# Kernel optimization log

Measured on AMD Instinct MI355X. Metric: run time of the kernel, lower is better.

Reference implementation:

```python
import jax, jax.numpy as jnp
import numpy as np

NUM_HEADS = 16


def setup_inputs() -> dict:
    key = jax.random.key(0)
    ks = jax.random.split(key, 7)
    B, S, H = 4, 2048, 1024
    scale = 1.0 / np.sqrt(H)
    return {
        "hidden_states": jax.random.normal(ks[0], (B, S, H), dtype=jnp.float32),
        "attention_mask": jnp.ones((B, S), dtype=jnp.int32),
        "Wq": jax.random.normal(ks[1], (H, H), dtype=jnp.float32) * scale,
        "bq": jnp.zeros((H,), dtype=jnp.float32),
        "Wk": jax.random.normal(ks[2], (H, H), dtype=jnp.float32) * scale,
        "bk": jnp.zeros((H,), dtype=jnp.float32),
        "Wv": jax.random.normal(ks[3], (H, H), dtype=jnp.float32) * scale,
        "bv": jnp.zeros((H,), dtype=jnp.float32),
    }


def _split_heads(x, n_heads):
    B, S, H = x.shape
    return x.reshape(B, S, n_heads, H // n_heads).transpose(0, 2, 1, 3)  # [B,h,S,d]


def reference(hidden_states, attention_mask, Wq, bq, Wk, bk, Wv, bv):
    B, S, H = hidden_states.shape
    dh = H // NUM_HEADS
    # nn.Linear applies x @ W.T + b
    q = _split_heads(hidden_states @ Wq.T + bq, NUM_HEADS)
    k = _split_heads(hidden_states @ Wk.T + bk, NUM_HEADS)
    v = _split_heads(hidden_states @ Wv.T + bv, NUM_HEADS)
    scores = jnp.einsum("bhqd,bhkd->bhqk", q, k)  # [B,h,S,S]
    # masked_fill with -inf before scaling == masking after scaling
    mask = attention_mask[:, None, None, :] == 0
    scores = jnp.where(mask, -jnp.inf, scores)
    probs = jax.nn.softmax(scores / jnp.sqrt(jnp.float32(dh)), axis=-1)
    out = jnp.einsum("bhqk,bhkd->bhqd", probs, v)  # [B,h,S,d]
    return out.transpose(0, 2, 1, 3).reshape(B, S, H)
```

## Files before the change

### kernel.cpp

```cpp
#include <hip/hip_runtime.h>
#include <hip/hip_bf16.h>
#include <stdint.h>

constexpr int CB  = 4;
constexpr int CS  = 2048;
constexpr int CH  = 1024;
constexpr int CNH = 16;
constexpr int CDH = 64;
constexpr int CM  = CB * CS;

typedef __bf16 bf16x8 __attribute__((ext_vector_type(8)));
typedef float  f32x4  __attribute__((ext_vector_type(4)));

__device__ __forceinline__ unsigned short f2bf(float f) {
    union { float f; unsigned u; } c; c.f = f;
    unsigned u = c.u;
    unsigned r = (u + 0x7fffu + ((u >> 16) & 1u)) >> 16;
    return (unsigned short)r;
}

__device__ __forceinline__ void gl_lds16(const void* g, void* l) {
    __builtin_amdgcn_global_load_lds((const __attribute__((address_space(1))) uint32_t*)g,
                                     (__attribute__((address_space(3))) uint32_t*)l,
                                     16, 0, 0);
}

__device__ __forceinline__ float fexp2(float x) {
#if __has_builtin(__builtin_amdgcn_exp2f)
    return __builtin_amdgcn_exp2f(x);
#else
    return exp2f(x);
#endif
}

__device__ __forceinline__ unsigned cvtpk_bf16(float lo, float hi) {
    unsigned r;
    asm("v_cvt_pk_bf16_f32 %0, %1, %2" : "=v"(r) : "v"(lo), "v"(hi));
    return r;
}

__device__ __forceinline__ void pl32swap(unsigned &a, unsigned &b) {
#if __has_builtin(__builtin_amdgcn_permlane32_swap)
    auto r = __builtin_amdgcn_permlane32_swap(a, b, false, false);
    a = r[0]; b = r[1];
#else
    int lane = threadIdx.x & 63;
    unsigned as = (unsigned)__shfl((int)a, lane ^ 32);
    unsigned bs = (unsigned)__shfl((int)b, lane ^ 32);
    unsigned na = (lane < 32) ? a : bs;
    unsigned nb = (lane < 32) ? as : b;
    a = na; b = nb;
#endif
}

__device__ __forceinline__ void pl16swap(unsigned &a, unsigned &b) {
#if __has_builtin(__builtin_amdgcn_permlane16_swap)
    auto r = __builtin_amdgcn_permlane16_swap(a, b, false, false);
    a = r[0]; b = r[1];
#else
    unsigned as = __builtin_amdgcn_ds_swizzle(a, 0x401F);
    unsigned bs = __builtin_amdgcn_ds_swizzle(b, 0x401F);
    int odd = (threadIdx.x >> 4) & 1;
    unsigned na = odd ? bs : a;
    unsigned nb = odd ? b : as;
    a = na; b = nb;
#endif
}

constexpr float C_SC = 0.125f * 1.44269504f;

__global__ __launch_bounds__(256) void cvt_all(const float* __restrict__ hs,
                                               const float* __restrict__ w0,
                                               const float* __restrict__ w1,
                                               const float* __restrict__ w2,
                                               unsigned short* __restrict__ Xb,
                                               unsigned short* __restrict__ Wb) {
    int z = blockIdx.y;
    const float* src; unsigned short* dst; int n4;
    if (z == 0)      { src = hs; dst = Xb;              n4 = CM * CH / 4; }
    else if (z == 1) { src = w0; dst = Wb;              n4 = CH * CH / 4; }
    else if (z == 2) { src = w1; dst = Wb + CH * CH;    n4 = CH * CH / 4; }
    else             { src = w2; dst = Wb + 2 * CH * CH; n4 = CH * CH / 4; }
    int i = blockIdx.x * blockDim.x + threadIdx.x;
    if (i < n4) {
        float4 v = ((const float4*)src)[i];
        ushort4 o;
        o.x = f2bf(v.x); o.y = f2bf(v.y); o.z = f2bf(v.z); o.w = f2bf(v.w);
        ((ushort4*)dst)[i] = o;
    }
}

__global__ __launch_bounds__(256) void qkv_gemm(
    const unsigned short* __restrict__ Xb,
    const unsigned short* __restrict__ Wb,
    const float* __restrict__ bq, const float* __restrict__ bk, const float* __restrict__ bv,
    unsigned short* __restrict__ Qo,
    unsigned short* __restrict__ Ko,
    unsigned short* __restrict__ Vt)
{
    __shared__ alignas(16) unsigned char smem[34816];
    typedef unsigned short (*tile_t)[128][32];
    tile_t As = (tile_t)smem;
    tile_t Bs = (tile_t)(smem + 16384);
    typedef unsigned short (*ep_t)[136];
    ep_t Ep = (ep_t)smem;

    const int tid  = threadIdx.x;
    const int wave = tid >> 6, lane = tid & 63;
    const int wm = wave >> 1, wn = wave & 1;
    const int col = lane & 15, quad = lane >> 4;
    const int gm = blockIdx.x * 128, gn = blockIdx.y * 128;
    const int z  = blockIdx.z;
    const unsigned short* W = Wb + (size_t)z * CH * CH;

    f32x4 zero = {0.f, 0.f, 0.f, 0.f};
    f32x4 acc[4][4];
    for (int i = 0; i < 4; i++) for (int j = 0; j < 4; j++) acc[i][j] = zero;

    const int arow = lane >> 2;
    const int acol = (lane & 3) * 8;

    auto stage = [&](int buf, int k0) {
        for (int c = 0; c < 2; ++c) {
            int r0 = wave * 32 + c * 16;
            gl_lds16(Xb + (size_t)(gm + r0 + arow) * CH + k0 + acol, &As[buf][r0][0]);
            gl_lds16(W  + (size_t)(gn + r0 + arow) * CH + k0 + acol, &Bs[buf][r0][0]);
        }
    };

    stage(0, 0);
    for (int kk = 0; kk < 32; ++kk) {
        int cur = kk & 1;
        __syncthreads();
        if (kk < 31) stage(cur ^ 1, (kk + 1) * 32);
        bf16x8 af[4], bfm[4];
        for (int i = 0; i < 4; i++)
            af[i] = *(const bf16x8*)&As[cur][wm * 64 + i * 16 + col][quad * 8];
        for (int j = 0; j < 4; j++)
            bfm[j] = *(const bf16x8*)&Bs[cur][wn * 64 + j * 16 + col][quad * 8];
        for (int i = 0; i < 4; i++)
            for (int j = 0; j < 4; j++)
                acc[i][j] = __builtin_amdgcn_mfma_f32_16x16x32_bf16(af[i], bfm[j], acc[i][j], 0, 0, 0);
    }

    __syncthreads();

    const float* bias = (z == 0) ? bq : (z == 1) ? bk : bv;
    const int bb = gm >> 11, ss0 = gm & 2047;
    const int h0 = gn >> 6;

    if (z == 2) {
        for (int j = 0; j < 4; j++) {
            int nl = wn * 64 + j * 16 + col;
            float bias_v = bias[gn + nl];
            for (int i = 0; i < 4; i++) {
                int ml = wm * 64 + i * 16 + quad * 4;
                unsigned d0 = (unsigned)f2bf(acc[i][j][0] + bias_v) |
                              ((unsigned)f2bf(acc[i][j][1] + bias_v) << 16);
                unsigned d1 = (unsigned)f2bf(acc[i][j][2] + bias_v) |
                              ((unsigned)f2bf(acc[i][j][3] + bias_v) << 16);
                *(unsigned*)&Ep[nl][ml]     = d0;
                *(unsigned*)&Ep[nl][ml + 2] = d1;
            }
        }
        __syncthreads();
        for (int p = 0; p < 8; p++) {
            int nl = p * 16 + (tid >> 4);
            int seg = tid & 15;
            uint4 v = *(const uint4*)&Ep[nl][seg * 8];
            int h = h0 + (nl >> 6), d = nl & 63;
            *(uint4*)(Vt + ((size_t)(bb * CNH + h) * CDH + d) * CS + ss0 + seg * 8) = v;
        }
    } else {
        const float mulf = (z == 0) ? C_SC : 1.0f;
        for (int j = 0; j < 4; j++) {
            int nl = wn * 64 + j * 16 + col;
            float bias_v = bias[gn + nl];
            for (int i = 0; i < 4; i++)
                for (int r = 0; r < 4; r++) {
                    int ml = wm * 64 + i * 16 + quad * 4 + r;
                    Ep[ml][nl] = f2bf((acc[i][j][r] + bias_v) * mulf);
                }
        }
        __syncthreads();
        unsigned short* dst01 = (z == 0) ? Qo : Ko;
        for (int p = 0; p < 8; p++) {
            int ml = p * 16 + (tid >> 4);
            int half = (tid >> 3) & 1, seg = tid & 7;
            uint4 v = *(const uint4*)&Ep[ml][half * 64 + seg * 8];
            int h = h0 + half;
            *(uint4*)(dst01 + ((size_t)(bb * CNH + h) * CS + ss0 + ml) * CDH + seg * 8) = v;
        }
    }
}

__global__ __launch_bounds__(256, 2) void flash_attn(
    const unsigned short* __restrict__ Q,
    const unsigned short* __restrict__ K,
    const unsigned short* __restrict__ Vt,
    const int* __restrict__ mask,
    float* __restrict__ out)
{
    __shared__ alignas(16) unsigned short Ks[2][64][64];
    __shared__ alignas(16) unsigned short Vs[2][64][64];
    __shared__ unsigned int Mbits[64];

    const int tid  = threadIdx.x;
    const int wave = tid >> 6, lane = tid & 63;
    const int col = lane & 15, quad = lane >> 4;
    const int bh = blockIdx.y;
    const int bI = bh >> 4, hI = bh & 15;
    const int q0 = blockIdx.x * 256 + wave * 64;

    const unsigned short* Qp = Q  + (size_t)bh * CS * CDH;
    const unsigned short* Kp = K  + (size_t)bh * CS * CDH;
    const unsigned short* Vp = Vt + (size_t)bh * CDH * CS;

    {
        const int* mg = mask + bI * CS;
        for (int j = 0; j < 8; j++) {
            int idx = wave * 512 + j * 64 + lane;
            unsigned long long bal = __ballot(mg[idx] != 0);
            if (lane == 0) {
                Mbits[wave * 16 + j * 2]     = (unsigned int)bal;
                Mbits[wave * 16 + j * 2 + 1] = (unsigned int)(bal >> 32);
            }
        }
    }

    bf16x8 aq[4][2];
    for (int i = 0; i < 4; i++)
        for (int ks = 0; ks < 2; ks++)
            aq[i][ks] = *(const bf16x8*)(Qp + (size_t)(q0 + i * 16 + col) * CDH + ks * 32 + quad * 8);

    bf16x8 onesb;
    {
        union { unsigned short u; __bf16 b; } ob; ob.u = 0x3F80;
        for (int j = 0; j < 8; j++) onesb[j] = ob.b;
    }

    f32x4 zero = {0.f, 0.f, 0.f, 0.f};
    f32x4 o[4][4], lfr[4];
    for (int i = 0; i < 4; i++) {
        lfr[i] = zero;
        for (int id = 0; id < 4; id++) o[i][id] = zero;
    }

    const int srow = lane >> 3;
    const int schk = (lane & 7) ^ srow;

    auto stageKV = [&](int buf, int t) {
        const unsigned short* kg = Kp + (size_t)t * 64 * CDH;
        for (int c = 0; c < 2; c++) {
            int r0 = wave * 16 + c * 8;
            gl_lds16(kg + (size_t)(r0 + srow) * CDH + schk * 8, &Ks[buf][r0][0]);
            gl_lds16(Vp + (size_t)(r0 + srow) * CS + t * 64 + schk * 8, &Vs[buf][r0][0]);
        }
    };

    stageKV(0, 0);
    for (int kt = 0; kt < 32; ++kt) {
        int cur = kt & 1;
        __syncthreads();
        if (kt < 31) stageKV(cur ^ 1, kt + 1);

        f32x4 sfr[4][4];
        for (int i = 0; i < 4; i++) for (int ik = 0; ik < 4; ik++) sfr[i][ik] = zero;
        for (int ks = 0; ks < 2; ks++) {
            bf16x8 bkf[4];
            for (int ik = 0; ik < 4; ik++)
                bkf[ik] = *(const bf16x8*)&Ks[cur][ik * 16 + col][((ks * 4 + quad) ^ (col & 7)) * 8];
            __builtin_amdgcn_s_setprio(1);
            for (int i = 0; i < 4; i++)
                for (int ik = 0; ik < 4; ik++)
                    sfr[i][ik] = __builtin_amdgcn_mfma_f32_16x16x32_bf16(bkf[ik], aq[i][ks], sfr[i][ik], 0, 0, 0);
            __builtin_amdgcn_s_setprio(0);
        }

        unsigned int w0 = Mbits[kt * 2], w1 = Mbits[kt * 2 + 1];
        if ((w0 & w1) != 0xFFFFFFFFu) {
            for (int ik = 0; ik < 4; ik++)
                for (int r = 0; r < 4; r++) {
                    int kv = ik * 16 + quad * 4 + r;
                    unsigned bit = (kv < 32) ? (w0 >> kv) : (w1 >> (kv - 32));
                    float madd = (bit & 1u) ? 0.f : -1.0e30f;
                    for (int i = 0; i < 4; i++) sfr[i][ik][r] += madd;
                }
        }

        bf16x8 bvf[2][4];
        for (int ks = 0; ks < 2; ks++)
            for (int id = 0; id < 4; id++)
                bvf[ks][id] = *(const bf16x8*)&Vs[cur][id * 16 + col][((ks * 4 + quad) ^ (col & 7)) * 8];

        for (int i = 0; i < 4; i++) {
            unsigned c[4][2];
            for (int ik = 0; ik < 4; ik++)
                for (int h = 0; h < 2; h++)
                    c[ik][h] = cvtpk_bf16(fexp2(sfr[i][ik][2 * h]), fexp2(sfr[i][ik][2 * h + 1]));

            unsigned a0 = c[0][0], b0 = c[1][0]; pl32swap(a0, b0); pl16swap(a0, b0);
            unsigned a1 = c[0][1], b1 = c[1][1]; pl32swap(a1, b1); pl16swap(a1, b1);
            unsigned a2 = c[2][0], b2 = c[3][0]; pl32swap(a2, b2); pl16swap(a2, b2);
            unsigned a3 = c[2][1], b3 = c[3][1]; pl32swap(a3, b3); pl16swap(a3, b3);

            uint4 lo4; lo4.x = a0; lo4.y = a1; lo4.z = b0; lo4.w = b1;
            uint4 hi4; hi4.x = a2; hi4.y = a3; hi4.z = b2; hi4.w = b3;
            bf16x8 ap0, ap1;
            __builtin_memcpy(&ap0, &lo4, 16);
            __builtin_memcpy(&ap1, &hi4, 16);

            __builtin_amdgcn_s_setprio(1);
            for (int id = 0; id < 4; id++)
                o[i][id] = __builtin_amdgcn_mfma_f32_16x16x32_bf16(ap0, bvf[0][id], o[i][id], 0, 0, 0);
            lfr[i] = __builtin_amdgcn_mfma_f32_16x16x32_bf16(ap0, onesb, lfr[i], 0, 0, 0);
            for (int id = 0; id < 4; id++)
                o[i][id] = __builtin_amdgcn_mfma_f32_16x16x32_bf16(ap1, bvf[1][id], o[i][id], 0, 0, 0);
            lfr[i] = __builtin_amdgcn_mfma_f32_16x16x32_bf16(ap1, onesb, lfr[i], 0, 0, 0);
            __builtin_amdgcn_s_setprio(0);
        }
    }

    for (int i = 0; i < 4; i++)
        for (int r = 0; r < 4; r++) {
            int sI = q0 + i * 16 + quad * 4 + r;
            float inv = 1.0f / lfr[i][r];
            for (int id = 0; id < 4; id++)
                out[((size_t)(bI * CS + sI)) * CH + hI * CDH + id * 16 + col] = o[i][id][r] * inv;
        }
}

extern "C" void kernel_launch(void* const* d_in, const int* in_sizes, int n_in,
                              void* d_out, int out_size, void* d_ws, size_t ws_size,
                              hipStream_t stream) {
    const float* hs  = (const float*)d_in[0];
    const int*  mask = (const int*)d_in[1];
    const float* Wq  = (const float*)d_in[2];
    const float* bq  = (const float*)d_in[3];
    const float* Wk  = (const float*)d_in[4];
    const float* bk  = (const float*)d_in[5];
    const float* Wv  = (const float*)d_in[6];
    const float* bv  = (const float*)d_in[7];
    float* out = (float*)d_out;

    char* ws = (char*)d_ws;
    unsigned short* Xb = (unsigned short*)(ws);
    unsigned short* Wb = (unsigned short*)(ws + 16777216);
    unsigned short* Qb = (unsigned short*)(ws + 23068672);
    unsigned short* Kb = (unsigned short*)(ws + 39845888);
    unsigned short* Vt = (unsigned short*)(ws + 56623104);

    cvt_all<<<dim3(8192, 4), 256, 0, stream>>>(hs, Wq, Wk, Wv, Xb, Wb);

    qkv_gemm<<<dim3(CM / 128, CH / 128, 3), 256, 0, stream>>>(Xb, Wb, bq, bk, bv, Qb, Kb, Vt);

    flash_attn<<<dim3(CS / 256, CB * CNH), 256, 0, stream>>>(Qb, Kb, Vt, mask, out);
}
```

Baseline: 253.6 us.

## Split KV range across two wave groups in flash attention and reduce partials via LDS

Flash attention blocks now run 512 threads: two groups of four waves each process half the KV sequence for the same 256 query rows, with separate double-buffered K/V tiles. After the loop, the partial output accumulators and row sums are exchanged through shared memory and summed, with each group writing half the head dimension. Block indices are also remapped so that consecutive workgroups are spread across heads, which may improve cache locality across XCDs. This doubles waves per query tile to raise occupancy and latency hiding, at the cost of more LDS (about 64KB per block), an extra reduction phase, and fewer blocks resident per CU.

```diff
diff --git a/kernel.cpp b/kernel.cpp
--- a/kernel.cpp
+++ b/kernel.cpp
@@ -186,31 +186,40 @@
         unsigned short* dst01 = (z == 0) ? Qo : Ko;
         for (int p = 0; p < 8; p++) {
             int ml = p * 16 + (tid >> 4);
-            int half = (tid >> 3) & 1, seg = tid & 7;
-            uint4 v = *(const uint4*)&Ep[ml][half * 64 + seg * 8];
-            int h = h0 + half;
+            int half2 = (tid >> 3) & 1, seg = tid & 7;
+            uint4 v = *(const uint4*)&Ep[ml][half2 * 64 + seg * 8];
+            int h = h0 + half2;
             *(uint4*)(dst01 + ((size_t)(bb * CNH + h) * CS + ss0 + ml) * CDH + seg * 8) = v;
         }
     }
 }
 
-__global__ __launch_bounds__(256, 2) void flash_attn(
+__global__ __launch_bounds__(512, 4) void flash_attn(
     const unsigned short* __restrict__ Q,
     const unsigned short* __restrict__ K,
     const unsigned short* __restrict__ Vt,
     const int* __restrict__ mask,
     float* __restrict__ out)
 {
-    __shared__ alignas(16) unsigned short Ks[2][64][64];
-    __shared__ alignas(16) unsigned short Vs[2][64][64];
-    __shared__ unsigned int Mbits[64];
+    __shared__ alignas(16) unsigned char smem[65792];
+    typedef unsigned short (*kv_t)[2][64][64];
+    kv_t Ks = (kv_t)smem;
+    kv_t Vs = (kv_t)(smem + 32768);
+    unsigned int* Mbits = (unsigned int*)(smem + 65536);
+    float* scr = (float*)smem;
 
     const int tid  = threadIdx.x;
     const int wave = tid >> 6, lane = tid & 63;
     const int col = lane & 15, quad = lane >> 4;
-    const int bh = blockIdx.y;
+    const int qg  = wave & 3;
+    const int kvh = wave >> 2;
+
+    const int wg   = blockIdx.y * gridDim.x + blockIdx.x;
+    const int nid  = (wg & 7) * 64 + (wg >> 3);
+    const int bh   = nid >> 3;
+    const int qblk = nid & 7;
     const int bI = bh >> 4, hI = bh & 15;
-    const int q0 = blockIdx.x * 256 + wave * 64;
+    const int q0 = qblk * 256 + qg * 64;
 
     const unsigned short* Qp = Q  + (size_t)bh * CS * CDH;
     const unsigned short* Kp = K  + (size_t)bh * CS * CDH;
@@ -218,12 +227,12 @@
 
     {
         const int* mg = mask + bI * CS;
-        for (int j = 0; j < 8; j++) {
-            int idx = wave * 512 + j * 64 + lane;
+        for (int j = 0; j < 4; j++) {
+            int idx = wave * 256 + j * 64 + lane;
             unsigned long long bal = __ballot(mg[idx] != 0);
             if (lane == 0) {
-                Mbits[wave * 16 + j * 2]     = (unsigned int)bal;
-                Mbits[wave * 16 + j * 2 + 1] = (unsigned int)(bal >> 32);
+                Mbits[(wave * 4 + j) * 2]     = (unsigned int)bal;
+                Mbits[(wave * 4 + j) * 2 + 1] = (unsigned int)(bal >> 32);
             }
         }
     }
@@ -250,26 +259,27 @@
     const int schk = (lane & 7) ^ srow;
 
     auto stageKV = [&](int buf, int t) {
-        const unsigned short* kg = Kp + (size_t)t * 64 * CDH;
+        int gt = kvh * 16 + t;
+        const unsigned short* kg = Kp + (size_t)gt * 64 * CDH;
         for (int c = 0; c < 2; c++) {
-            int r0 = wave * 16 + c * 8;
-            gl_lds16(kg + (size_t)(r0 + srow) * CDH + schk * 8, &Ks[buf][r0][0]);
-            gl_lds16(Vp + (size_t)(r0 + srow) * CS + t * 64 + schk * 8, &Vs[buf][r0][0]);
+            int r0 = qg * 16 + c * 8;
+            gl_lds16(kg + (size_t)(r0 + srow) * CDH + schk * 8, &Ks[kvh][buf][r0][0]);
+            gl_lds16(Vp + (size_t)(r0 + srow) * CS + gt * 64 + schk * 8, &Vs[kvh][buf][r0][0]);
         }
     };
 
     stageKV(0, 0);
-    for (int kt = 0; kt < 32; ++kt) {
+    for (int kt = 0; kt < 16; ++kt) {
         int cur = kt & 1;
         __syncthreads();
-        if (kt < 31) stageKV(cur ^ 1, kt + 1);
+        if (kt < 15) stageKV(cur ^ 1, kt + 1);
 
         f32x4 sfr[4][4];
         for (int i = 0; i < 4; i++) for (int ik = 0; ik < 4; ik++) sfr[i][ik] = zero;
         for (int ks = 0; ks < 2; ks++) {
             bf16x8 bkf[4];
             for (int ik = 0; ik < 4; ik++)
-                bkf[ik] = *(const bf16x8*)&Ks[cur][ik * 16 + col][((ks * 4 + quad) ^ (col & 7)) * 8];
+                bkf[ik] = *(const bf16x8*)&Ks[kvh][cur][ik * 16 + col][((ks * 4 + quad) ^ (col & 7)) * 8];
             __builtin_amdgcn_s_setprio(1);
             for (int i = 0; i < 4; i++)
                 for (int ik = 0; ik < 4; ik++)
@@ -277,7 +287,8 @@
             __builtin_amdgcn_s_setprio(0);
         }
 
-        unsigned int w0 = Mbits[kt * 2], w1 = Mbits[kt * 2 + 1];
+        int gt = kvh * 16 + kt;
+        unsigned int w0 = Mbits[gt * 2], w1 = Mbits[gt * 2 + 1];
         if ((w0 & w1) != 0xFFFFFFFFu) {
             for (int ik = 0; ik < 4; ik++)
                 for (int r = 0; r < 4; r++) {
@@ -291,7 +302,7 @@
         bf16x8 bvf[2][4];
         for (int ks = 0; ks < 2; ks++)
             for (int id = 0; id < 4; id++)
-                bvf[ks][id] = *(const bf16x8*)&Vs[cur][id * 16 + col][((ks * 4 + quad) ^ (col & 7)) * 8];
+                bvf[ks][id] = *(const bf16x8*)&Vs[kvh][cur][id * 16 + col][((ks * 4 + quad) ^ (col & 7)) * 8];
 
         for (int i = 0; i < 4; i++) {
             unsigned c[4][2];
@@ -321,12 +332,37 @@
         }
     }
 
+    __syncthreads();
+    const int ownb = kvh * 2;
+    const int notb = 2 - ownb;
+    const int pw   = wave ^ 4;
+
+    for (int i = 0; i < 4; i++)
+        for (int j2 = 0; j2 < 2; j2++)
+            *(f32x4*)&scr[(((wave * 4 + i) * 2 + j2) * 64 + lane) * 4] = o[i][notb + j2];
+    __syncthreads();
+    for (int i = 0; i < 4; i++)
+        for (int j2 = 0; j2 < 2; j2++) {
+            f32x4 p = *(const f32x4*)&scr[(((pw * 4 + i) * 2 + j2) * 64 + lane) * 4];
+            o[i][ownb + j2] += p;
+        }
+    __syncthreads();
+    for (int i = 0; i < 4; i++)
+        *(f32x4*)&scr[((wave * 4 + i) * 64 + lane) * 4] = lfr[i];
+    __syncthreads();
+    for (int i = 0; i < 4; i++) {
+        f32x4 p = *(const f32x4*)&scr[((pw * 4 + i) * 64 + lane) * 4];
+        lfr[i] += p;
+    }
+
     for (int i = 0; i < 4; i++)
         for (int r = 0; r < 4; r++) {
             int sI = q0 + i * 16 + quad * 4 + r;
             float inv = 1.0f / lfr[i][r];
-            for (int id = 0; id < 4; id++)
+            for (int j2 = 0; j2 < 2; j2++) {
+                int id = ownb + j2;
                 out[((size_t)(bI * CS + sI)) * CH + hI * CDH + id * 16 + col] = o[i][id][r] * inv;
+            }
         }
 }
 
@@ -354,5 +390,5 @@
 
     qkv_gemm<<<dim3(CM / 128, CH / 128, 3), 256, 0, stream>>>(Xb, Wb, bq, bk, bv, Qb, Kb, Vt);
 
-    flash_attn<<<dim3(CS / 256, CB * CNH), 256, 0, stream>>>(Qb, Kb, Vt, mask, out);
-}
+    flash_attn<<<dim3(8, 64), 512, 0, stream>>>(Qb, Kb, Vt, mask, out);
+}
```

Result: slower. 699.9 us (+176.0%).
